# Optimization experiments

Measured on AMD Instinct MI355X. Metric: run time of the kernel, lower is better.

Reference implementation:

```python
import jax, jax.numpy as jnp
import numpy as np

NEG_SLOPE = 0.2


def _attn_layer(x, src, dst, W, a, n_nodes):
    # x: (N, Cin), W: (Cout, Cin) torch Linear convention, a: (2*Cout,)
    h = x @ W.T                                  # (N, Cout)
    H = h.shape[-1]
    # cat([x_i, x_j]) @ a  ==  h[dst] @ a[:H] + h[src] @ a[H:]
    s_i = h @ a[:H]                              # (N,)
    s_j = h @ a[H:]                              # (N,)
    score = s_i[dst] + s_j[src]                  # (E,)
    alpha = jax.nn.leaky_relu(score, NEG_SLOPE)
    # segment softmax over destination nodes
    amax = jax.ops.segment_max(alpha, dst, num_segments=n_nodes)
    amax = jnp.where(jnp.isfinite(amax), amax, 0.0)
    ex = jnp.exp(alpha - amax[dst])
    denom = jax.ops.segment_sum(ex, dst, num_segments=n_nodes)
    alpha = ex / denom[dst]                      # (E,)
    msg = h[src] * alpha[:, None]                # (E, Cout)
    sums = jax.ops.segment_sum(msg, dst, num_segments=n_nodes)
    cnt = jax.ops.segment_sum(jnp.ones_like(alpha), dst, num_segments=n_nodes)
    return sums / jnp.maximum(cnt, 1.0)[:, None]  # mean aggregation


def setup_inputs() -> dict:
    key = jax.random.key(0)
    ks = jax.random.split(key, 8)
    B, N, C, H, E = 16, 2048, 256, 256, 262144
    NT = B * N
    temporal_features = jax.random.normal(ks[0], (B, N, C), dtype=jnp.float32)
    edge_index = jax.random.randint(ks[1], (2, E), 0, NT, dtype=jnp.int64)
    sc = 1.0 / np.sqrt(C)
    W1 = jax.random.normal(ks[2], (H, C), dtype=jnp.float32) * sc
    a1 = jax.random.normal(ks[3], (2 * H,), dtype=jnp.float32) * sc
    W2 = jax.random.normal(ks[4], (H, H), dtype=jnp.float32) * sc
    a2 = jax.random.normal(ks[5], (2 * H,), dtype=jnp.float32) * sc
    W3 = jax.random.normal(ks[6], (H, H), dtype=jnp.float32) * sc
    a3 = jax.random.normal(ks[7], (2 * H,), dtype=jnp.float32) * sc
    return {"temporal_features": temporal_features, "edge_index": edge_index,
            "W1": W1, "a1": a1, "W2": W2, "a2": a2, "W3": W3, "a3": a3}


def reference(temporal_features, edge_index, W1, a1, W2, a2, W3, a3):
    B, N, C = temporal_features.shape
    n_nodes = B * N
    src, dst = edge_index[0], edge_index[1]  # x_j = x[src], x_i = x[dst]
    x = temporal_features.reshape(n_nodes, C)
    for W, a in ((W1, a1), (W2, a2), (W3, a3)):
        x = _attn_layer(x, src, dst, W, a, n_nodes)
        x = jax.nn.elu(x)
    return x.reshape(B, N, -1)
```

## Files before the change

### kernel.cpp

```cpp
#include <hip/hip_runtime.h>
#include <math.h>
#include <stdint.h>


typedef float f32x4 __attribute__((ext_vector_type(4)));
typedef _Float16 f16x8 __attribute__((ext_vector_type(8)));
typedef _Float16 f16x4 __attribute__((ext_vector_type(4)));


__global__ __launch_bounds__(256) void convert_f16(const float* __restrict__ src,
                                                   _Float16* __restrict__ dstp)
{
    const int i = (blockIdx.x * 256 + threadIdx.x) * 8;
    float4 a = *(const float4*)&src[i];
    float4 b = *(const float4*)&src[i + 4];
    f16x8 o = {(_Float16)a.x, (_Float16)a.y, (_Float16)a.z, (_Float16)a.w,
               (_Float16)b.x, (_Float16)b.y, (_Float16)b.z, (_Float16)b.w};
    *(f16x8*)&dstp[i] = o;
}


__global__ __launch_bounds__(512, 2) void gemm_f16(const _Float16* __restrict__ X,
                                                   const _Float16* __restrict__ Wh,
                                                   const float* __restrict__ avec,
                                                   _Float16* __restrict__ Hout,
                                                   float* __restrict__ si,
                                                   float* __restrict__ sj)
{
    __shared__ float Es[16][260];

    const int tid  = threadIdx.x;
    const int lane = tid & 63;
    const int w    = tid >> 6;
    const int ln   = lane & 15;
    const int kq   = lane >> 4;
    const int m0   = blockIdx.x * 128;

    f16x8 wf[2][8];
#pragma unroll
    for (int ks = 0; ks < 8; ++ks)
#pragma unroll
        for (int j = 0; j < 2; ++j)
            wf[j][ks] = *(const f16x8*)&Wh[(size_t)(w * 32 + j * 16 + ln) * 256 + ks * 32 + kq * 8];

    f32x4 acc[8][2] = {};
    const _Float16* Xb = X + (size_t)m0 * 256 + kq * 8;

    f16x8 xf[8];
#pragma unroll
    for (int i = 0; i < 8; ++i)
        xf[i] = *(const f16x8*)&Xb[(size_t)(i * 16 + ln) * 256];

#pragma unroll
    for (int ks = 0; ks < 8; ++ks) {
        f16x8 xn[8];
        if (ks < 7) {
#pragma unroll
            for (int i = 0; i < 8; ++i)
                xn[i] = *(const f16x8*)&Xb[(size_t)(i * 16 + ln) * 256 + (ks + 1) * 32];
        }
#pragma unroll
        for (int i = 0; i < 8; ++i)
#pragma unroll
            for (int j = 0; j < 2; ++j)
                acc[i][j] = __builtin_amdgcn_mfma_f32_16x16x32_f16(xf[i], wf[j][ks], acc[i][j], 0, 0, 0);
        if (ks < 7) {
#pragma unroll
            for (int i = 0; i < 8; ++i) xf[i] = xn[i];
        }
    }

    const int er = tid >> 5;
    const int ec = tid & 31;
    for (int i = 0; i < 8; ++i) {
#pragma unroll
        for (int j = 0; j < 2; ++j) {
            const int col = w * 32 + j * 16 + ln;
#pragma unroll
            for (int q = 0; q < 4; ++q)
                Es[kq * 4 + q][col] = acc[i][j][q];
        }
        __syncthreads();
        const int grow = m0 + i * 16 + er;
        const int c0 = ec * 8;
        f32x4 v0 = *(const f32x4*)&Es[er][c0];
        f32x4 v1 = *(const f32x4*)&Es[er][c0 + 4];
        f16x8 ho = {(_Float16)v0[0], (_Float16)v0[1], (_Float16)v0[2], (_Float16)v0[3],
                    (_Float16)v1[0], (_Float16)v1[1], (_Float16)v1[2], (_Float16)v1[3]};
        *(f16x8*)&Hout[(size_t)grow * 256 + c0] = ho;

        f32x4 al0 = *(const f32x4*)&avec[c0];
        f32x4 al1 = *(const f32x4*)&avec[c0 + 4];
        f32x4 ah0 = *(const f32x4*)&avec[256 + c0];
        f32x4 ah1 = *(const f32x4*)&avec[256 + c0 + 4];
        float d0 = v0[0]*al0[0] + v0[1]*al0[1] + v0[2]*al0[2] + v0[3]*al0[3]
                 + v1[0]*al1[0] + v1[1]*al1[1] + v1[2]*al1[2] + v1[3]*al1[3];
        float d1 = v0[0]*ah0[0] + v0[1]*ah0[1] + v0[2]*ah0[2] + v0[3]*ah0[3]
                 + v1[0]*ah1[0] + v1[1]*ah1[1] + v1[2]*ah1[2] + v1[3]*ah1[3];
#pragma unroll
        for (int d = 16; d; d >>= 1) {
            d0 += __shfl_xor(d0, d);
            d1 += __shfl_xor(d1, d);
        }
        if (ec == 0) { si[grow] = d0; sj[grow] = d1; }
        __syncthreads();
    }
}


__global__ void zero_int(int* p, int n)
{
    int i = blockIdx.x * blockDim.x + threadIdx.x;
    if (i < n) p[i] = 0;
}

__global__ void hist_kernel(const int* __restrict__ dst, int* __restrict__ cnt, int E)
{
    int e = blockIdx.x * blockDim.x + threadIdx.x;
    if (e < E) atomicAdd(&cnt[dst[e]], 1);
}

__global__ __launch_bounds__(1024) void scan_part(const int* __restrict__ cnt,
                                                  int* __restrict__ off,
                                                  int* __restrict__ bsum)
{
    __shared__ int buf[1024];
    const int tid = threadIdx.x;
    const int g = blockIdx.x * 1024 + tid;
    int v = cnt[g];
    buf[tid] = v;
    __syncthreads();
#pragma unroll
    for (int d = 1; d < 1024; d <<= 1) {
        int t = (tid >= d) ? buf[tid - d] : 0;
        __syncthreads();
        buf[tid] += t;
        __syncthreads();
    }
    off[g] = buf[tid] - v;
    if (tid == 1023) bsum[blockIdx.x] = buf[1023];
}

__global__ void scan_bsum(int* bsum, int nb)
{
    __shared__ int b[64];
    const int tid = threadIdx.x;
    b[tid] = (tid < nb) ? bsum[tid] : 0;
    __syncthreads();
    if (tid == 0) {
        int a = 0;
        for (int i = 0; i < nb; ++i) { int t = b[i]; b[i] = a; a += t; }
    }
    __syncthreads();
    if (tid < nb) bsum[tid] = b[tid];
}

__global__ __launch_bounds__(1024) void scan_add(const int* __restrict__ bsum,
                                                 int* __restrict__ off,
                                                 int* __restrict__ cursor,
                                                 int NT, int E)
{
    const int tid = threadIdx.x;
    const int g = blockIdx.x * 1024 + tid;
    int v = off[g] + bsum[blockIdx.x];
    off[g] = v;
    cursor[g] = v;
    if (g == 0) off[NT] = E;
}

__global__ void scatter_kernel(const int* __restrict__ src,
                               const int* __restrict__ dst,
                               int* __restrict__ cursor,
                               int* __restrict__ ssrc, int E)
{
    int e = blockIdx.x * blockDim.x + threadIdx.x;
    if (e < E) {
        int p = atomicAdd(&cursor[dst[e]], 1);
        ssrc[p] = src[e];
    }
}


__device__ __forceinline__ float bcast_f(float x, int l)
{
    return __uint_as_float(__builtin_amdgcn_readlane(__float_as_uint(x), l));
}

template <int F16OUT>
__global__ __launch_bounds__(256) void aggregate(const _Float16* __restrict__ Hh,
                                                 const float* __restrict__ si,
                                                 const float* __restrict__ sj,
                                                 const int* __restrict__ off,
                                                 const int* __restrict__ ssrc,
                                                 void* __restrict__ outv,
                                                 int n_nodes)
{
    const int v = (blockIdx.x * 256 + threadIdx.x) >> 6;
    const int lane = threadIdx.x & 63;
    if (v >= n_nodes) return;

    const int e0 = off[v], e1 = off[v + 1];
    const int deg = e1 - e0;
    f32x4 acc = {0.f, 0.f, 0.f, 0.f};

    if (deg > 0 && deg <= 64) {
        const float siv = si[v];
        const int idx = e0 + lane;
        const bool on = idx < e1;
        int s = 0;
        float scv = -1e30f;
        if (on) {
            s = ssrc[idx];
            float t = siv + sj[s];
            scv = (t >= 0.f) ? t : 0.2f * t;
        }
        float m = scv;
#pragma unroll
        for (int d = 32; d; d >>= 1) m = fmaxf(m, __shfl_xor(m, d));
        float wv = on ? __expf(scv - m) : 0.f;
        float den = wv;
#pragma unroll
        for (int d = 32; d; d >>= 1) den += __shfl_xor(den, d);

        const int c4 = lane * 4;
        for (int eo = 0; eo < deg; eo += 4) {
            const int l1 = (eo + 1 < 63) ? eo + 1 : 63;
            const int l2 = (eo + 2 < 63) ? eo + 2 : 63;
            const int l3 = (eo + 3 < 63) ? eo + 3 : 63;
            const int s0 = __builtin_amdgcn_readlane(s, eo);
            const int s1 = __builtin_amdgcn_readlane(s, l1);
            const int s2 = __builtin_amdgcn_readlane(s, l2);
            const int s3 = __builtin_amdgcn_readlane(s, l3);
            const float w0 = bcast_f(wv, eo);
            const float w1 = bcast_f(wv, l1);
            const float w2 = bcast_f(wv, l2);
            const float w3 = bcast_f(wv, l3);
            const f16x4 v0 = *(const f16x4*)&Hh[(size_t)s0 * 256 + c4];
            const f16x4 v1 = *(const f16x4*)&Hh[(size_t)s1 * 256 + c4];
            const f16x4 v2 = *(const f16x4*)&Hh[(size_t)s2 * 256 + c4];
            const f16x4 v3 = *(const f16x4*)&Hh[(size_t)s3 * 256 + c4];
#pragma unroll
            for (int q = 0; q < 4; ++q)
                acc[q] += w0 * (float)v0[q] + w1 * (float)v1[q]
                        + w2 * (float)v2[q] + w3 * (float)v3[q];
        }
        const float inv = 1.f / (den * (float)deg);
#pragma unroll
        for (int q = 0; q < 4; ++q) acc[q] *= inv;
    } else if (deg > 64) {
        const float siv = si[v];
        float m = -1e30f;
        for (int b = e0 + lane; b < e1; b += 64) {
            float t = siv + sj[ssrc[b]];
            t = (t >= 0.f) ? t : 0.2f * t;
            m = fmaxf(m, t);
        }
#pragma unroll
        for (int d = 32; d; d >>= 1) m = fmaxf(m, __shfl_xor(m, d));
        float den = 0.f;
        for (int b = e0 + lane; b < e1; b += 64) {
            float t = siv + sj[ssrc[b]];
            t = (t >= 0.f) ? t : 0.2f * t;
            den += __expf(t - m);
        }
#pragma unroll
        for (int d = 32; d; d >>= 1) den += __shfl_xor(den, d);
        for (int e = e0; e < e1; ++e) {
            const int s = ssrc[e];
            float t = siv + sj[s];
            t = (t >= 0.f) ? t : 0.2f * t;
            const float wgt = __expf(t - m);
            const f16x4 hv = *(const f16x4*)&Hh[(size_t)s * 256 + lane * 4];
#pragma unroll
            for (int q = 0; q < 4; ++q) acc[q] += wgt * (float)hv[q];
        }
        const float inv = 1.f / (den * (float)deg);
#pragma unroll
        for (int q = 0; q < 4; ++q) acc[q] *= inv;
    }

    float4 o;
    o.x = (acc[0] > 0.f) ? acc[0] : (__expf(acc[0]) - 1.f);
    o.y = (acc[1] > 0.f) ? acc[1] : (__expf(acc[1]) - 1.f);
    o.z = (acc[2] > 0.f) ? acc[2] : (__expf(acc[2]) - 1.f);
    o.w = (acc[3] > 0.f) ? acc[3] : (__expf(acc[3]) - 1.f);
    if (F16OUT) {
        f16x4 oh = {(_Float16)o.x, (_Float16)o.y, (_Float16)o.z, (_Float16)o.w};
        *(f16x4*)&((_Float16*)outv)[(size_t)v * 256 + lane * 4] = oh;
    } else {
        *(float4*)&((float*)outv)[(size_t)v * 256 + lane * 4] = o;
    }
}


extern "C" void kernel_launch(void* const* d_in, const int* in_sizes, int n_in,
                              void* d_out, int out_size, void* d_ws, size_t ws_size,
                              hipStream_t stream)
{
    const float* x0 = (const float*)d_in[0];
    const int*   ei = (const int*)d_in[1];
    const float* Ws[3] = {(const float*)d_in[2], (const float*)d_in[4], (const float*)d_in[6]};
    const float* as[3] = {(const float*)d_in[3], (const float*)d_in[5], (const float*)d_in[7]};
    float* out = (float*)d_out;

    const int NT = in_sizes[0] / 256;
    const int E  = in_sizes[1] / 2;
    const int* srcI = ei;
    const int* dstI = ei + E;

    _Float16* Hh = (_Float16*)d_ws;
    _Float16* Xh = Hh + (size_t)NT * 256;
    float* si    = (float*)(Xh + (size_t)NT * 256);
    float* sj    = si + NT;
    int* cnt     = (int*)(sj + NT);
    int* off     = cnt + NT;
    int* cursor  = off + NT + 1;
    int* ssrc    = cursor + NT;
    int* bsum    = ssrc + E;
    _Float16* Wh = (_Float16*)(((uintptr_t)(bsum + 64) + 255) & ~(uintptr_t)255);

    for (int l = 0; l < 3; ++l)
        convert_f16<<<32, 256, 0, stream>>>(Ws[l], Wh + (size_t)l * 65536);
    convert_f16<<<NT * 256 / 2048, 256, 0, stream>>>(x0, Xh);

    zero_int<<<(NT + 255) / 256, 256, 0, stream>>>(cnt, NT);
    hist_kernel<<<(E + 255) / 256, 256, 0, stream>>>(dstI, cnt, E);
    scan_part<<<NT / 1024, 1024, 0, stream>>>(cnt, off, bsum);
    scan_bsum<<<1, 64, 0, stream>>>(bsum, NT / 1024);
    scan_add<<<NT / 1024, 1024, 0, stream>>>(bsum, off, cursor, NT, E);
    scatter_kernel<<<(E + 255) / 256, 256, 0, stream>>>(srcI, dstI, cursor, ssrc, E);

    for (int l = 0; l < 3; ++l) {
        gemm_f16<<<NT / 128, 512, 0, stream>>>(Xh, Wh + (size_t)l * 65536, as[l], Hh, si, sj);
        if (l < 2)
            aggregate<1><<<NT / 4, 256, 0, stream>>>(Hh, si, sj, off, ssrc, (void*)Xh, NT);
        else
            aggregate<0><<<NT / 4, 256, 0, stream>>>(Hh, si, sj, off, ssrc, (void*)out, NT);
    }
}
```

Before: 282.4 us.

## Stage GEMM tiles in swizzled LDS with 2x4 warp tiling

Replaces the register-resident weight fragments and direct global X loads in the projection GEMM with cooperative staging of X and W k-slices into XOR-swizzled shared memory. Each of the 8 waves now computes a 64x64 sub-tile instead of 128x32, so global fragments are reused across waves. The epilogue is adapted so each row group is written by the owning wave row. The trade-offs are extra barriers per k-step, no prefetch of the next slice, and a larger 48 KB shared allocation, with the launch bound no longer requesting 2 blocks per CU.

```diff
diff --git a/kernel.cpp b/kernel.cpp
--- a/kernel.cpp
+++ b/kernel.cpp
@@ -20,68 +20,94 @@
 }
 
 
-__global__ __launch_bounds__(512, 2) void gemm_f16(const _Float16* __restrict__ X,
-                                                   const _Float16* __restrict__ Wh,
-                                                   const float* __restrict__ avec,
-                                                   _Float16* __restrict__ Hout,
-                                                   float* __restrict__ si,
-                                                   float* __restrict__ sj)
-{
-    __shared__ float Es[16][260];
+#define SWZ(row, byte) ((byte) ^ (((row) & 7) << 4))
+
+__global__ __launch_bounds__(512) void gemm_f16(const _Float16* __restrict__ X,
+                                                const _Float16* __restrict__ Wh,
+                                                const float* __restrict__ avec,
+                                                _Float16* __restrict__ Hout,
+                                                float* __restrict__ si,
+                                                float* __restrict__ sj)
+{
+    __shared__ __align__(16) unsigned char smem[49152];
+    char* Xs = (char*)smem;
+    char* Wl = (char*)smem + 16384;
+    float (*Es)[260] = (float (*)[260])smem;
 
     const int tid  = threadIdx.x;
     const int lane = tid & 63;
     const int w    = tid >> 6;
+    const int wr   = w >> 2;
+    const int wc   = w & 3;
     const int ln   = lane & 15;
     const int kq   = lane >> 4;
     const int m0   = blockIdx.x * 128;
 
-    f16x8 wf[2][8];
-#pragma unroll
-    for (int ks = 0; ks < 8; ++ks)
-#pragma unroll
-        for (int j = 0; j < 2; ++j)
-            wf[j][ks] = *(const f16x8*)&Wh[(size_t)(w * 32 + j * 16 + ln) * 256 + ks * 32 + kq * 8];
-
-    f32x4 acc[8][2] = {};
-    const _Float16* Xb = X + (size_t)m0 * 256 + kq * 8;
-
-    f16x8 xf[8];
-#pragma unroll
-    for (int i = 0; i < 8; ++i)
-        xf[i] = *(const f16x8*)&Xb[(size_t)(i * 16 + ln) * 256];
-
-#pragma unroll
-    for (int ks = 0; ks < 8; ++ks) {
-        f16x8 xn[8];
-        if (ks < 7) {
-#pragma unroll
-            for (int i = 0; i < 8; ++i)
-                xn[i] = *(const f16x8*)&Xb[(size_t)(i * 16 + ln) * 256 + (ks + 1) * 32];
-        }
-#pragma unroll
-        for (int i = 0; i < 8; ++i)
-#pragma unroll
-            for (int j = 0; j < 2; ++j)
-                acc[i][j] = __builtin_amdgcn_mfma_f32_16x16x32_f16(xf[i], wf[j][ks], acc[i][j], 0, 0, 0);
-        if (ks < 7) {
-#pragma unroll
-            for (int i = 0; i < 8; ++i) xf[i] = xn[i];
-        }
+    const int xr = tid >> 2;
+    const int xc = tid & 3;
+    const int wrow = tid >> 1;
+    const int wcb  = (tid & 1) * 64;
+
+    const _Float16* Xg = X  + (size_t)(m0 + xr) * 256 + xc * 16;
+    const _Float16* Wg = Wh + (size_t)wrow * 256 + wcb / 2;
+    char* XsW = Xs + SWZ(xr, xr * 128 + xc * 32);
+    char* XsW2 = Xs + SWZ(xr, xr * 128 + xc * 32 + 16);
+    char* WlW0 = Wl + SWZ(wrow, wrow * 128 + wcb + 0);
+    char* WlW1 = Wl + SWZ(wrow, wrow * 128 + wcb + 16);
+    char* WlW2 = Wl + SWZ(wrow, wrow * 128 + wcb + 32);
+    char* WlW3 = Wl + SWZ(wrow, wrow * 128 + wcb + 48);
+
+    f32x4 acc[4][4] = {};
+
+    for (int k0 = 0; k0 < 256; k0 += 64) {
+        f16x8 x0 = *(const f16x8*)&Xg[k0];
+        f16x8 x1 = *(const f16x8*)&Xg[k0 + 8];
+        f16x8 w0 = *(const f16x8*)&Wg[k0];
+        f16x8 w1 = *(const f16x8*)&Wg[k0 + 8];
+        f16x8 w2 = *(const f16x8*)&Wg[k0 + 16];
+        f16x8 w3 = *(const f16x8*)&Wg[k0 + 24];
+        *(f16x8*)XsW  = x0;  *(f16x8*)XsW2 = x1;
+        *(f16x8*)WlW0 = w0;  *(f16x8*)WlW1 = w1;
+        *(f16x8*)WlW2 = w2;  *(f16x8*)WlW3 = w3;
+        __syncthreads();
+
+#pragma unroll
+        for (int kk = 0; kk < 2; ++kk) {
+            f16x8 af[4], bf[4];
+#pragma unroll
+            for (int i = 0; i < 4; ++i) {
+                const int row = wr * 64 + i * 16 + ln;
+                af[i] = *(const f16x8*)(Xs + SWZ(row, row * 128 + kk * 64 + kq * 16));
+            }
+#pragma unroll
+            for (int j = 0; j < 4; ++j) {
+                const int row = wc * 64 + j * 16 + ln;
+                bf[j] = *(const f16x8*)(Wl + SWZ(row, row * 128 + kk * 64 + kq * 16));
+            }
+#pragma unroll
+            for (int i = 0; i < 4; ++i)
+#pragma unroll
+                for (int j = 0; j < 4; ++j)
+                    acc[i][j] = __builtin_amdgcn_mfma_f32_16x16x32_f16(af[i], bf[j], acc[i][j], 0, 0, 0);
+        }
+        __syncthreads();
     }
 
     const int er = tid >> 5;
     const int ec = tid & 31;
-    for (int i = 0; i < 8; ++i) {
-#pragma unroll
-        for (int j = 0; j < 2; ++j) {
-            const int col = w * 32 + j * 16 + ln;
-#pragma unroll
-            for (int q = 0; q < 4; ++q)
-                Es[kq * 4 + q][col] = acc[i][j][q];
-        }
-        __syncthreads();
-        const int grow = m0 + i * 16 + er;
+    for (int g = 0; g < 8; ++g) {
+        if (wr == (g >> 2)) {
+            const int i = g & 3;
+#pragma unroll
+            for (int j = 0; j < 4; ++j) {
+                const int col = wc * 64 + j * 16 + ln;
+#pragma unroll
+                for (int q = 0; q < 4; ++q)
+                    Es[kq * 4 + q][col] = acc[i][j][q];
+            }
+        }
+        __syncthreads();
+        const int grow = m0 + g * 16 + er;
         const int c0 = ec * 8;
         f32x4 v0 = *(const f32x4*)&Es[er][c0];
         f32x4 v1 = *(const f32x4*)&Es[er][c0 + 4];
```

After: 249.0 us. 1.13x faster.
